# Kernel tuning notes

Measured on AMD Instinct MI355X. Metric: run time of the kernel, lower is better.

The kernel has to match this reference:

```python
import jax, jax.numpy as jnp
import numpy as np

H = 768   # encoder hidden size
NH = 4    # boundary attention heads
HD = H // NH
E = 9     # ent_type_size
R = 12    # rel_type_size
D = 64    # inner_dim
B = 4
S = 1024


def setup_inputs() -> dict:
    key = jax.random.key(0)
    ks = jax.random.split(key, 8)
    n = lambda k, shp: jax.random.normal(k, shp, jnp.float32) * 0.02
    return dict(
        hidden_states=jax.random.normal(ks[0], (B, S, H), jnp.float32),
        attention_mask=jnp.ones((B, S), jnp.float32),
        in_proj_w=n(ks[1], (3 * H, H)), in_proj_b=jnp.zeros((3 * H,), jnp.float32),
        out_proj_w=n(ks[2], (H, H)), out_proj_b=jnp.zeros((H,), jnp.float32),
        gate_w=n(ks[3], (H, H)), gate_b=jnp.zeros((H,), jnp.float32),
        ln_g=jnp.ones((H,), jnp.float32), ln_b=jnp.zeros((H,), jnp.float32),
        ent_w=n(ks[4], (E * 2 * D, H)), ent_b=jnp.zeros((E * 2 * D,), jnp.float32),
        prior_w=n(ks[5], (H, E)), prior_b=jnp.zeros((H,), jnp.float32),
        rel_w=n(ks[6], (R * 2 * D, 2 * H)), rel_b=jnp.zeros((R * 2 * D,), jnp.float32),
    )


def _sinusoidal_pos_emb(seq_len, dim, dtype):
    pos = jnp.arange(seq_len, dtype=dtype)[:, None]                 # [S,1]
    inv = jnp.power(jnp.asarray(10000.0, dtype), -2.0 * jnp.arange(dim // 2, dtype=dtype) / dim)
    ang = pos * inv                                                  # [S,D/2]
    emb = jnp.stack([jnp.sin(ang), jnp.cos(ang)], axis=-1).reshape(seq_len, dim)  # [sin0,cos0,sin1,cos1,...]
    return emb


def _gp_matrix(hs, W, b, mask):
    # hs: [B,S,Hin], W: [T*2D, Hin], mask: [B,S]
    bsz, seq_len, _ = hs.shape
    out = hs @ W.T + b                                               # [B,S,T*2D]
    T = out.shape[-1] // (2 * D)
    out = out.reshape(bsz, seq_len, T, 2 * D)
    qw, kw = out[..., :D], out[..., D:]                              # [B,S,T,D]
    # RoPE
    pe = _sinusoidal_pos_emb(seq_len, D, hs.dtype)                   # [S,D]
    cos = jnp.repeat(pe[:, 1::2], 2, axis=-1)[None, :, None, :]      # [1,S,1,D]
    sin = jnp.repeat(pe[:, ::2], 2, axis=-1)[None, :, None, :]

    def rot(x):
        x2 = jnp.stack([-x[..., 1::2], x[..., ::2]], axis=-1).reshape(x.shape)
        return x * cos + x2 * sin

    qw, kw = rot(qw), rot(kw)
    logits = jnp.einsum('bmtd,bntd->btmn', qw, kw)                   # [B,T,S,S]
    pad = mask[:, None, None, :]                                     # masks key dim
    logits = logits * pad - (1.0 - pad) * 1e12
    tril = jnp.tril(jnp.ones((seq_len, seq_len), logits.dtype), -1)
    logits = logits - tril * 1e12                                    # strictly lower triangle masked
    return logits / jnp.sqrt(jnp.asarray(D, logits.dtype))


def _boundary_attention(hs, mask, in_proj_w, in_proj_b, out_proj_w, out_proj_b,
                        gate_w, gate_b, ln_g, ln_b):
    bsz, seq_len, _ = hs.shape
    qkv = hs @ in_proj_w.T + in_proj_b                               # [B,S,3H]
    q, k, v = jnp.split(qkv, 3, axis=-1)
    q = q.reshape(bsz, seq_len, NH, HD)
    k = k.reshape(bsz, seq_len, NH, HD)
    v = v.reshape(bsz, seq_len, NH, HD)
    scores = jnp.einsum('bqhd,bkhd->bhqk', q, k) / jnp.sqrt(jnp.asarray(HD, hs.dtype))
    key_pad = (mask == 0)[:, None, None, :]                          # [B,1,1,S]
    scores = jnp.where(key_pad, jnp.asarray(-1e9, hs.dtype), scores)
    attn = jax.nn.softmax(scores, axis=-1)
    ctx = jnp.einsum('bhqk,bkhd->bqhd', attn, v).reshape(bsz, seq_len, H)
    attn_out = ctx @ out_proj_w.T + out_proj_b
    gate = jax.nn.sigmoid(attn_out @ gate_w.T + gate_b)
    x = hs + gate * attn_out
    mu = jnp.mean(x, axis=-1, keepdims=True)
    var = jnp.var(x, axis=-1, keepdims=True)
    return (x - mu) / jnp.sqrt(var + 1e-5) * ln_g + ln_b


def reference(hidden_states, attention_mask, in_proj_w, in_proj_b, out_proj_w, out_proj_b,
              gate_w, gate_b, ln_g, ln_b, ent_w, ent_b, prior_w, prior_b, rel_w, rel_b):
    enhanced = _boundary_attention(hidden_states, attention_mask, in_proj_w, in_proj_b,
                                   out_proj_w, out_proj_b, gate_w, gate_b, ln_g, ln_b)
    ent_logits = _gp_matrix(enhanced, ent_w, ent_b, attention_mask)  # [B,E,S,S]
    ent_prior = jnp.max(ent_logits, axis=-1)                          # [B,E,S]
    ent_prior = jnp.swapaxes(ent_prior, 1, 2)                         # [B,S,E]
    prior_feat = jax.nn.relu(ent_prior @ prior_w.T + prior_b)         # [B,S,H]
    rel_hidden = jnp.concatenate([enhanced, prior_feat], axis=-1)     # [B,S,2H]
    rel_logits = _gp_matrix(rel_hidden, rel_w, rel_b, attention_mask) # [B,R,S,S]
    return (ent_logits, rel_logits, enhanced)
```

## Files before the change

kernel.cpp:

```cpp
#include <hip/hip_runtime.h>
#include <math.h>

#define H_   768
#define NH_  4
#define HD_  192
#define E_   9
#define R_   12
#define D_   64
#define B_   4
#define S_   1024
#define H3_  (3 * H_)
#define MBS_ (B_ * S_)

typedef unsigned short u16;
typedef __attribute__((ext_vector_type(4))) int   i32x4;
typedef __attribute__((ext_vector_type(4))) float f32x4;
typedef __attribute__((ext_vector_type(8))) unsigned short u16x8;

static const long OUT_REL_OFF = (long)B_ * E_ * S_ * S_;
static const long OUT_ENH_OFF = OUT_REL_OFF + (long)B_ * R_ * S_ * S_;

__device__ __forceinline__ u16 f2bf(float f) {
    unsigned u = __builtin_bit_cast(unsigned, f);
    return (u16)((u + 0x7fffu + ((u >> 16) & 1u)) >> 16);
}
__device__ __forceinline__ float bf2f(u16 h) {
    return __builtin_bit_cast(float, (unsigned)h << 16);
}
__device__ __forceinline__ void gload16(const u16* g, u16* l) {
    __builtin_amdgcn_global_load_lds(
        (__attribute__((address_space(1))) void*)g,
        (__attribute__((address_space(3))) void*)l, 16, 0, 0);
}
__device__ __forceinline__ void mfma_bf16(f32x4& acc, i32x4 a, i32x4 b) {
    asm volatile("v_mfma_f32_16x16x32_bf16 %0, %1, %2, %0"
                 : "+v"(acc) : "v"(a), "v"(b));
}

template<int BM, int BN, int EPI, int OBF, int NS>
__global__ __launch_bounds__(256) void gemm_mfma(
    const u16* __restrict__ A, const u16* __restrict__ Bw,
    const float* __restrict__ bias, void* __restrict__ Cv,
    int K, int lda, int ldb, int ldc, int nh,
    long sAb, long sAh, long sBb, long sBh, long sCb, long sCh,
    const float* __restrict__ mask, float scale, float* __restrict__ aux)
{
    constexpr int MI = BM / 32, NJ = BN / 32;
    constexpr int BUFE = (BM + BN) * 64;
    const int z = blockIdx.z;
    const int zb = z / nh, zh = z - zb * nh;
    A  += zb * sAb + zh * sAh;
    Bw += zb * sBb + zh * sBh;

    const int gx = gridDim.x, gy = gridDim.y;
    int id = blockIdx.y * gx + blockIdx.x;
    const int nwg = gx * gy;
    if ((nwg & 7) == 0) id = (id & 7) * (nwg >> 3) + (id >> 3);
    const int bx = id % gx, by = id / gx;
    const int m0 = by * BM, n0 = bx * BN;

    __shared__ u16 lds[NS * BUFE];

    const int t = threadIdx.x;
    const int lane = t & 63, wid = t >> 6;
    const int wr = wid >> 1, wc = wid & 1;
    const int l16 = lane & 15, l4 = lane >> 4;

    auto stage = [&](int kt, int buf) {
        u16* la = lds + buf * BUFE;
        u16* lb = la + BM * 64;
        const int k0 = kt << 6;
        #pragma unroll
        for (int i = 0; i < BM / 32; ++i) {
            const int e = i * 256 + t;
            const int row = e >> 3;
            const int c = ((e & 7) ^ (row & 7)) << 3;
            gload16(A + (long)(m0 + row) * lda + k0 + c, la + e * 8);
        }
        #pragma unroll
        for (int i = 0; i < BN / 32; ++i) {
            const int e = i * 256 + t;
            const int row = e >> 3;
            const int c = ((e & 7) ^ (row & 7)) << 3;
            gload16(Bw + (long)(n0 + row) * ldb + k0 + c, lb + e * 8);
        }
    };

    f32x4 acc[MI][NJ];
    #pragma unroll
    for (int mi = 0; mi < MI; ++mi)
        #pragma unroll
        for (int nj = 0; nj < NJ; ++nj)
            #pragma unroll
            for (int q = 0; q < 4; ++q) acc[mi][nj][q] = 0.0f;

    const int nt = K >> 6;
    stage(0, 0);
    __syncthreads();
    for (int tt = 0; tt < nt; ++tt) {
        const int cur = (NS == 2) ? (tt & 1) : 0;
        if (NS == 2 && tt + 1 < nt) stage(tt + 1, cur ^ 1);
        const u16* la = lds + cur * BUFE;
        const u16* lb = la + BM * 64;
        i32x4 af[MI][2], bfr[NJ][2];
        #pragma unroll
        for (int mi = 0; mi < MI; ++mi)
            #pragma unroll
            for (int kk = 0; kk < 2; ++kk) {
                const int row = wr * (BM / 2) + mi * 16 + l16;
                af[mi][kk] = *(const i32x4*)&la[row * 64 + ((((kk << 2) + l4) ^ (row & 7)) << 3)];
            }
        #pragma unroll
        for (int nj = 0; nj < NJ; ++nj)
            #pragma unroll
            for (int kk = 0; kk < 2; ++kk) {
                const int row = wc * (BN / 2) + nj * 16 + l16;
                bfr[nj][kk] = *(const i32x4*)&lb[row * 64 + ((((kk << 2) + l4) ^ (row & 7)) << 3)];
            }
        #pragma unroll
        for (int kk = 0; kk < 2; ++kk)
            #pragma unroll
            for (int mi = 0; mi < MI; ++mi)
                #pragma unroll
                for (int nj = 0; nj < NJ; ++nj)
                    mfma_bf16(acc[mi][nj], af[mi][kk], bfr[nj][kk]);
        __syncthreads();
    }
    __builtin_amdgcn_sched_barrier(0);
    asm volatile("s_nop 7");
    asm volatile("s_nop 7");
    __builtin_amdgcn_sched_barrier(0);

    if (EPI == 1 || EPI == 3 || EPI == 5) mask += (long)zb * S_;
    const long cbase = zb * sCb + zh * sCh;

    float* sminv = (float*)lds;
    if (EPI == 6) {
        if (t < BM) {
            const float* pp = aux + ((long)z * S_ + m0 + t) * 16;
            float s = 0.0f;
            #pragma unroll
            for (int i = 0; i < 16; ++i) s += pp[i];
            sminv[t] = 1.0f / s;
        }
        __syncthreads();
    }

    float red[MI][4];
    if (EPI == 3 || EPI == 5) {
        #pragma unroll
        for (int mi = 0; mi < MI; ++mi)
            #pragma unroll
            for (int r = 0; r < 4; ++r) red[mi][r] = (EPI == 3) ? -INFINITY : 0.0f;
    }

    #pragma unroll
    for (int mi = 0; mi < MI; ++mi) {
        #pragma unroll
        for (int nj = 0; nj < NJ; ++nj) {
            const int gn = n0 + wc * (BN / 2) + nj * 16 + l16;
            const float bv = ((EPI == 0 || EPI == 4) && bias) ? bias[gn] : 0.0f;
            float invf = 0.0f;
            if (EPI == 4) invf = exp2f(-(float)((gn & 63) >> 1) * 0.41524101186092503f);
            #pragma unroll
            for (int r = 0; r < 4; ++r) {
                const int gm = m0 + wr * (BM / 2) + mi * 16 + l4 * 4 + r;
                float v = acc[mi][nj][r];
                const long cidx = cbase + (long)gm * ldc + gn;
                if (EPI == 0) {
                    v += bv;
                    if (OBF) ((u16*)Cv)[cidx] = f2bf(v);
                    else     ((float*)Cv)[cidx] = v;
                } else if (EPI == 1 || EPI == 3) {
                    const float pad = mask[gn];
                    v = v * pad - (1.0f - pad) * 1e12f;
                    if (gm > gn) v -= 1e12f;
                    v *= 0.125f;
                    ((float*)Cv)[cidx] = v;
                    if (EPI == 3) red[mi][r] = fmaxf(red[mi][r], v);
                } else if (EPI == 5) {
                    float tv = 0.0f;
                    if (mask[gn] != 0.0f) tv = __expf(v * scale);
                    ((u16*)Cv)[cidx] = f2bf(tv);
                    red[mi][r] += tv;
                } else if (EPI == 6) {
                    v *= sminv[gm - m0];
                    ((u16*)Cv)[cidx] = f2bf(v);
                } else {
                    v += bv;
                    const int sp = gm & (S_ - 1);
                    float sn, cs;
                    __sincosf((float)sp * invf, &sn, &cs);
                    const float pv = __shfl_xor(v, 1, 64);
                    v = (gn & 1) ? fmaf(v, cs, pv * sn) : fmaf(v, cs, -pv * sn);
                    ((u16*)Cv)[cidx] = f2bf(v);
                }
            }
        }
    }

    if (EPI == 3 || EPI == 5) {
        #pragma unroll
        for (int mi = 0; mi < MI; ++mi) {
            #pragma unroll
            for (int r = 0; r < 4; ++r) {
                float m = red[mi][r];
                if (EPI == 3) {
                    m = fmaxf(m, __shfl_xor(m, 1, 64));
                    m = fmaxf(m, __shfl_xor(m, 2, 64));
                    m = fmaxf(m, __shfl_xor(m, 4, 64));
                    m = fmaxf(m, __shfl_xor(m, 8, 64));
                } else {
                    m += __shfl_xor(m, 1, 64);
                    m += __shfl_xor(m, 2, 64);
                    m += __shfl_xor(m, 4, 64);
                    m += __shfl_xor(m, 8, 64);
                }
                if (l16 == 0) {
                    const int gm = m0 + wr * (BM / 2) + mi * 16 + l4 * 4 + r;
                    aux[((long)z * S_ + gm) * 16 + bx * 2 + wc] = m;
                }
            }
        }
    }
}

__global__ __launch_bounds__(256) void cast_all(
    const float* __restrict__ hs, const float* __restrict__ ipw,
    const float* __restrict__ opw, const float* __restrict__ gw,
    const float* __restrict__ entw, const float* __restrict__ relw,
    u16* hs_o, u16* ipw_o, u16* opw_o, u16* gw_o, u16* entw_o, u16* relw_o)
{
    const int blk = blockIdx.x;
    const float* in; u16* out; long base;
    if      (blk < 3072) { in = hs;   out = hs_o;   base = (long)blk * 1024; }
    else if (blk < 4800) { in = ipw;  out = ipw_o;  base = (long)(blk - 3072) * 1024; }
    else if (blk < 5376) { in = opw;  out = opw_o;  base = (long)(blk - 4800) * 1024; }
    else if (blk < 5952) { in = gw;   out = gw_o;   base = (long)(blk - 5376) * 1024; }
    else if (blk < 6816) { in = entw; out = entw_o; base = (long)(blk - 5952) * 1024; }
    else                 { in = relw; out = relw_o; base = (long)(blk - 6816) * 1024; }
    const long idx = base + (long)threadIdx.x * 4;
    const float4 v = *(const float4*)&in[idx];
    ushort4 o; o.x = f2bf(v.x); o.y = f2bf(v.y); o.z = f2bf(v.z); o.w = f2bf(v.w);
    *(ushort4*)&out[idx] = o;
}

__global__ __launch_bounds__(256) void transpose_v(
    const u16* __restrict__ qkv, u16* __restrict__ vt)
{
    __shared__ u16 tile[64][72];
    const int z = blockIdx.z, b = z >> 2, h = z & 3;
    const int d0 = blockIdx.x * 64, s0 = blockIdx.y * 64;
    const int t = threadIdx.x;
    const int r = t >> 2, c = (t & 3) << 4;
    const u16* src = qkv + ((long)(b * S_ + s0 + r)) * H3_ + 2 * H_ + h * HD_ + d0 + c;
    *(u16x8*)&tile[r][c]     = *(const u16x8*)src;
    *(u16x8*)&tile[r][c + 8] = *(const u16x8*)(src + 8);
    __syncthreads();
    u16 tmp[16];
    #pragma unroll
    for (int i = 0; i < 16; ++i) tmp[i] = tile[c + i][r];
    u16* dst = vt + ((long)z * HD_ + d0 + r) * S_ + s0 + c;
    *(u16x8*)dst       = *(u16x8*)&tmp[0];
    *(u16x8*)(dst + 8) = *(u16x8*)&tmp[8];
}

__global__ __launch_bounds__(256) void gate_ln_bf(
    const float* __restrict__ hs, const u16* __restrict__ aogl,
    const float* __restrict__ g, const float* __restrict__ bta,
    float* __restrict__ enh, u16* __restrict__ relh)
{
    const long row = blockIdx.x;
    const float* hrow = hs + row * H_;
    const u16* arow = aogl + row * (2 * H_);
    const int tid = threadIdx.x;
    float x[3];
    float sum = 0.0f, sq = 0.0f;
    #pragma unroll
    for (int i = 0; i < 3; ++i) {
        const int j = tid + i * 256;
        const float a = bf2f(arow[j]);
        const float gt = 1.0f / (1.0f + __expf(-bf2f(arow[H_ + j])));
        const float xv = hrow[j] + gt * a;
        x[i] = xv; sum += xv; sq += xv * xv;
    }
    __shared__ float sm[8];
    #pragma unroll
    for (int o = 32; o > 0; o >>= 1) {
        sum += __shfl_xor(sum, o, 64);
        sq  += __shfl_xor(sq, o, 64);
    }
    const int lane = tid & 63, wid = tid >> 6;
    if (lane == 0) { sm[wid] = sum; sm[4 + wid] = sq; }
    __syncthreads();
    sum = sm[0] + sm[1] + sm[2] + sm[3];
    sq  = sm[4] + sm[5] + sm[6] + sm[7];
    const float mu = sum * (1.0f / (float)H_);
    float var = sq * (1.0f / (float)H_) - mu * mu;
    var = fmaxf(var, 0.0f);
    const float inv = 1.0f / sqrtf(var + 1e-5f);
    #pragma unroll
    for (int i = 0; i < 3; ++i) {
        const int j = tid + i * 256;
        const float o = (x[i] - mu) * inv * g[j] + bta[j];
        enh[row * H_ + j] = o;
        relh[row * (2 * H_) + j] = f2bf(o);
    }
}

__global__ __launch_bounds__(256) void prior_fused(
    const float* __restrict__ pmax, const float* __restrict__ pw,
    const float* __restrict__ pb, u16* __restrict__ relh)
{
    const int row = blockIdx.x;
    const int b = row >> 10, m = row & (S_ - 1);
    __shared__ float pr[E_];
    const int tid = threadIdx.x;
    if (tid < E_) {
        const float* pp = pmax + ((long)(b * E_ + tid) * S_ + m) * 16;
        float mx = -INFINITY;
        #pragma unroll
        for (int i = 0; i < 16; ++i) mx = fmaxf(mx, pp[i]);
        pr[tid] = mx;
    }
    __syncthreads();
    float p[E_];
    #pragma unroll
    for (int e = 0; e < E_; ++e) p[e] = pr[e];
    u16* orow = relh + (long)row * (2 * H_) + H_;
    #pragma unroll
    for (int i = 0; i < 3; ++i) {
        const int j = tid + i * 256;
        float a = pb[j];
        #pragma unroll
        for (int e = 0; e < E_; ++e) a = fmaf(p[e], pw[j * E_ + e], a);
        orow[j] = f2bf(fmaxf(a, 0.0f));
    }
}

extern "C" void kernel_launch(void* const* d_in, const int* in_sizes, int n_in,
                              void* d_out, int out_size, void* d_ws, size_t ws_size,
                              hipStream_t stream)
{
    const float* hs   = (const float*)d_in[0];
    const float* mask = (const float*)d_in[1];
    const float* ipw  = (const float*)d_in[2];
    const float* ipb  = (const float*)d_in[3];
    const float* opw  = (const float*)d_in[4];
    const float* opb  = (const float*)d_in[5];
    const float* gw   = (const float*)d_in[6];
    const float* gb   = (const float*)d_in[7];
    const float* lng  = (const float*)d_in[8];
    const float* lnb  = (const float*)d_in[9];
    const float* entw = (const float*)d_in[10];
    const float* entb = (const float*)d_in[11];
    const float* prw  = (const float*)d_in[12];
    const float* prb  = (const float*)d_in[13];
    const float* relw = (const float*)d_in[14];
    const float* relb = (const float*)d_in[15];
    float* out = (float*)d_out;
    char* base = (char*)d_ws;

    u16* ipw_bf  = (u16*)(base + 0);
    u16* opw_bf  = (u16*)(base + 3538944);
    u16* gw_bf   = (u16*)(base + 4718592);
    u16* entw_bf = (u16*)(base + 5898240);
    u16* relw_bf = (u16*)(base + 7667712);
    u16* hs_bf   = (u16*)(base + 12386304);
    u16* qkv_bf  = (u16*)(base + 18677760);
    u16* vt_bf   = (u16*)(base + 37552128);
    u16* sc_bf   = (u16*)(base + 43843584);
    u16* ctx_bf  = (u16*)(base + 77398016);
    u16* aogl_bf = (u16*)(base + 83689472);
    float* bias2 = (float*)(base + 96272384);
    float* psum  = (float*)(base + 96280576);
    float* pmax  = (float*)(base + 97329152);
    u16* relh_bf = (u16*)(base + 18677760);
    u16* projr   = (u16*)(base + 37552128);
    float* enh   = out + OUT_ENH_OFF;

    const float qscale = 0.07216878364870323f;

    hipMemcpyAsync(bias2, opb, H_ * sizeof(float), hipMemcpyDeviceToDevice, stream);
    hipMemcpyAsync(bias2 + H_, gb, H_ * sizeof(float), hipMemcpyDeviceToDevice, stream);

    cast_all<<<9120, 256, 0, stream>>>(hs, ipw, opw, gw, entw, relw,
                                       hs_bf, ipw_bf, opw_bf, gw_bf, entw_bf, relw_bf);

    gemm_mfma<128,128,0,1,2><<<dim3(18, 32, 1), 256, 0, stream>>>(
        hs_bf, ipw_bf, ipb, qkv_bf, H_, H_, H_, H3_, 1,
        0,0,0,0,0,0, nullptr, 0.0f, nullptr);

    transpose_v<<<dim3(3, 16, 16), 256, 0, stream>>>(qkv_bf, vt_bf);

    gemm_mfma<128,128,5,1,2><<<dim3(8, 8, B_ * NH_), 256, 0, stream>>>(
        qkv_bf, qkv_bf + H_, nullptr, sc_bf, HD_, H3_, H3_, S_, NH_,
        (long)S_ * H3_, HD_, (long)S_ * H3_, HD_,
        (long)NH_ * S_ * S_, (long)S_ * S_, mask, qscale, psum);

    gemm_mfma<128,64,6,1,2><<<dim3(3, 8, B_ * NH_), 256, 0, stream>>>(
        sc_bf, vt_bf, nullptr, ctx_bf, S_, S_, S_, H_, NH_,
        (long)NH_ * S_ * S_, (long)S_ * S_, (long)NH_ * HD_ * S_, (long)HD_ * S_,
        (long)S_ * H_, HD_, nullptr, 0.0f, psum);

    gemm_mfma<128,128,0,1,2><<<dim3(12, 32, 1), 256, 0, stream>>>(
        ctx_bf, opw_bf, bias2, aogl_bf, H_, H_, H_, 2 * H_, 1,
        0,0,0,0,0,0, nullptr, 0.0f, nullptr);

    gate_ln_bf<<<MBS_, 256, 0, stream>>>(hs, aogl_bf, lng, lnb, enh, relh_bf);

    gemm_mfma<128,128,4,1,2><<<dim3(9, 32, 1), 256, 0, stream>>>(
        relh_bf, entw_bf, entb, projr, H_, 2 * H_, H_, E_ * 2 * D_, 1,
        0,0,0,0,0,0, nullptr, 0.0f, nullptr);

    gemm_mfma<128,128,3,0,1><<<dim3(8, 8, B_ * E_), 256, 0, stream>>>(
        projr, projr + D_, nullptr, out, D_, E_ * 2 * D_, E_ * 2 * D_, S_, E_,
        (long)S_ * E_ * 2 * D_, 2 * D_, (long)S_ * E_ * 2 * D_, 2 * D_,
        (long)E_ * S_ * S_, (long)S_ * S_, mask, 0.0f, pmax);

    prior_fused<<<MBS_, 256, 0, stream>>>(pmax, prw, prb, relh_bf);

    gemm_mfma<128,128,4,1,2><<<dim3(12, 32, 1), 256, 0, stream>>>(
        relh_bf, relw_bf, relb, projr, 2 * H_, 2 * H_, 2 * H_, R_ * 2 * D_, 1,
        0,0,0,0,0,0, nullptr, 0.0f, nullptr);

    gemm_mfma<128,128,1,0,1><<<dim3(8, 8, B_ * R_), 256, 0, stream>>>(
        projr, projr + D_, nullptr, out + OUT_REL_OFF, D_, R_ * 2 * D_, R_ * 2 * D_, S_, R_,
        (long)S_ * R_ * 2 * D_, 2 * D_, (long)S_ * R_ * 2 * D_, 2 * D_,
        (long)R_ * S_ * S_, (long)S_ * S_, mask, 0.0f, nullptr);

    (void)in_sizes; (void)n_in; (void)out_size; (void)ws_size;
}
```

Baseline: 256.4 us.

## Pipeline GEMM loads with vmcnt waits, fuse V transpose, retile GEMMs

Replaces the double-buffered GEMM main loop with a prefetch-two-ahead pipeline. It uses explicit vmcnt waits and raw barriers, so global-to-LDS loads overlap MFMA work. For K=64 GEMMs it adds a single-tile path with no loop. The V transpose kernel is removed and its work moves into the QKV projection epilogue, which writes V transposed through scattered stores. Several GEMMs switch to 128x96 or 64x96 tiles to give more workgroups, at the cost of smaller tiles and uncoalesced transposed writes.

```diff
diff --git a/kernel.cpp b/kernel.cpp
--- a/kernel.cpp
+++ b/kernel.cpp
@@ -15,7 +15,6 @@
 typedef unsigned short u16;
 typedef __attribute__((ext_vector_type(4))) int   i32x4;
 typedef __attribute__((ext_vector_type(4))) float f32x4;
-typedef __attribute__((ext_vector_type(8))) unsigned short u16x8;
 
 static const long OUT_REL_OFF = (long)B_ * E_ * S_ * S_;
 static const long OUT_ENH_OFF = OUT_REL_OFF + (long)B_ * R_ * S_ * S_;
@@ -37,7 +36,7 @@
                  : "+v"(acc) : "v"(a), "v"(b));
 }
 
-template<int BM, int BN, int EPI, int OBF, int NS>
+template<int BM, int BN, int EPI, int OBF, int PIPE>
 __global__ __launch_bounds__(256) void gemm_mfma(
     const u16* __restrict__ A, const u16* __restrict__ Bw,
     const float* __restrict__ bias, void* __restrict__ Cv,
@@ -47,6 +46,7 @@
 {
     constexpr int MI = BM / 32, NJ = BN / 32;
     constexpr int BUFE = (BM + BN) * 64;
+    constexpr int LPS  = BM / 32 + BN / 32;
     const int z = blockIdx.z;
     const int zb = z / nh, zh = z - zb * nh;
     A  += zb * sAb + zh * sAh;
@@ -59,15 +59,14 @@
     const int bx = id % gx, by = id / gx;
     const int m0 = by * BM, n0 = bx * BN;
 
-    __shared__ u16 lds[NS * BUFE];
+    __shared__ u16 lds[(PIPE ? 2 : 1) * BUFE];
 
     const int t = threadIdx.x;
     const int lane = t & 63, wid = t >> 6;
     const int wr = wid >> 1, wc = wid & 1;
     const int l16 = lane & 15, l4 = lane >> 4;
 
-    auto stage = [&](int kt, int buf) {
-        u16* la = lds + buf * BUFE;
+    auto stage = [&](int kt, u16* la) {
         u16* lb = la + BM * 64;
         const int k0 = kt << 6;
         #pragma unroll
@@ -95,13 +94,12 @@
             for (int q = 0; q < 4; ++q) acc[mi][nj][q] = 0.0f;
 
     const int nt = K >> 6;
-    stage(0, 0);
-    __syncthreads();
-    for (int tt = 0; tt < nt; ++tt) {
-        const int cur = (NS == 2) ? (tt & 1) : 0;
-        if (NS == 2 && tt + 1 < nt) stage(tt + 1, cur ^ 1);
-        const u16* la = lds + cur * BUFE;
-        const u16* lb = la + BM * 64;
+
+    if (PIPE == 0) {
+        stage(0, lds);
+        __syncthreads();
+        const u16* la = lds;
+        const u16* lb = lds + BM * 64;
         i32x4 af[MI][2], bfr[NJ][2];
         #pragma unroll
         for (int mi = 0; mi < MI; ++mi)
@@ -124,6 +122,48 @@
                 #pragma unroll
                 for (int nj = 0; nj < NJ; ++nj)
                     mfma_bf16(acc[mi][nj], af[mi][kk], bfr[nj][kk]);
+    } else {
+        stage(0, lds);
+        if (nt > 1) stage(1, lds + BUFE);
+        for (int tt = 0; tt < nt; ++tt) {
+            if (tt + 1 < nt) {
+                if constexpr (LPS == 8) asm volatile("s_waitcnt vmcnt(8)" ::: "memory");
+                else if constexpr (LPS == 7) asm volatile("s_waitcnt vmcnt(7)" ::: "memory");
+                else if constexpr (LPS == 6) asm volatile("s_waitcnt vmcnt(6)" ::: "memory");
+                else asm volatile("s_waitcnt vmcnt(5)" ::: "memory");
+            } else {
+                asm volatile("s_waitcnt vmcnt(0)" ::: "memory");
+            }
+            __builtin_amdgcn_s_barrier();
+            u16* la = lds + (tt & 1) * BUFE;
+            const u16* lb = la + BM * 64;
+            i32x4 af[MI][2], bfr[NJ][2];
+            #pragma unroll
+            for (int mi = 0; mi < MI; ++mi)
+                #pragma unroll
+                for (int kk = 0; kk < 2; ++kk) {
+                    const int row = wr * (BM / 2) + mi * 16 + l16;
+                    af[mi][kk] = *(const i32x4*)&la[row * 64 + ((((kk << 2) + l4) ^ (row & 7)) << 3)];
+                }
+            #pragma unroll
+            for (int nj = 0; nj < NJ; ++nj)
+                #pragma unroll
+                for (int kk = 0; kk < 2; ++kk) {
+                    const int row = wc * (BN / 2) + nj * 16 + l16;
+                    bfr[nj][kk] = *(const i32x4*)&lb[row * 64 + ((((kk << 2) + l4) ^ (row & 7)) << 3)];
+                }
+            asm volatile("s_waitcnt lgkmcnt(0)" ::: "memory");
+            __builtin_amdgcn_sched_barrier(0);
+            __builtin_amdgcn_s_barrier();
+            if (tt + 2 < nt) stage(tt + 2, la);
+            #pragma unroll
+            for (int kk = 0; kk < 2; ++kk)
+                #pragma unroll
+                for (int mi = 0; mi < MI; ++mi)
+                    #pragma unroll
+                    for (int nj = 0; nj < NJ; ++nj)
+                        mfma_bf16(acc[mi][nj], af[mi][kk], bfr[nj][kk]);
+        }
         __syncthreads();
     }
     __builtin_amdgcn_sched_barrier(0);
@@ -159,7 +199,7 @@
         #pragma unroll
         for (int nj = 0; nj < NJ; ++nj) {
             const int gn = n0 + wc * (BN / 2) + nj * 16 + l16;
-            const float bv = ((EPI == 0 || EPI == 4) && bias) ? bias[gn] : 0.0f;
+            const float bv = ((EPI == 0 || EPI == 4 || EPI == 7) && bias) ? bias[gn] : 0.0f;
             float invf = 0.0f;
             if (EPI == 4) invf = exp2f(-(float)((gn & 63) >> 1) * 0.41524101186092503f);
             #pragma unroll
@@ -171,6 +211,16 @@
                     v += bv;
                     if (OBF) ((u16*)Cv)[cidx] = f2bf(v);
                     else     ((float*)Cv)[cidx] = v;
+                } else if (EPI == 7) {
+                    v += bv;
+                    const u16 bfv = f2bf(v);
+                    ((u16*)Cv)[cidx] = bfv;
+                    if (gn >= 2 * H_) {
+                        const int hh = (gn - 2 * H_) / HD_;
+                        const int dd = (gn - 2 * H_) - hh * HD_;
+                        const int bb = gm >> 10, ss = gm & (S_ - 1);
+                        ((u16*)aux)[((long)(bb * NH_ + hh) * HD_ + dd) * S_ + ss] = bfv;
+                    }
                 } else if (EPI == 1 || EPI == 3) {
                     const float pad = mask[gn];
                     v = v * pad - (1.0f - pad) * 1e12f;
@@ -245,26 +295,6 @@
     *(ushort4*)&out[idx] = o;
 }
 
-__global__ __launch_bounds__(256) void transpose_v(
-    const u16* __restrict__ qkv, u16* __restrict__ vt)
-{
-    __shared__ u16 tile[64][72];
-    const int z = blockIdx.z, b = z >> 2, h = z & 3;
-    const int d0 = blockIdx.x * 64, s0 = blockIdx.y * 64;
-    const int t = threadIdx.x;
-    const int r = t >> 2, c = (t & 3) << 4;
-    const u16* src = qkv + ((long)(b * S_ + s0 + r)) * H3_ + 2 * H_ + h * HD_ + d0 + c;
-    *(u16x8*)&tile[r][c]     = *(const u16x8*)src;
-    *(u16x8*)&tile[r][c + 8] = *(const u16x8*)(src + 8);
-    __syncthreads();
-    u16 tmp[16];
-    #pragma unroll
-    for (int i = 0; i < 16; ++i) tmp[i] = tile[c + i][r];
-    u16* dst = vt + ((long)z * HD_ + d0 + r) * S_ + s0 + c;
-    *(u16x8*)dst       = *(u16x8*)&tmp[0];
-    *(u16x8*)(dst + 8) = *(u16x8*)&tmp[8];
-}
-
 __global__ __launch_bounds__(256) void gate_ln_bf(
     const float* __restrict__ hs, const u16* __restrict__ aogl,
     const float* __restrict__ g, const float* __restrict__ bta,
@@ -346,9 +376,7 @@
     const float* mask = (const float*)d_in[1];
     const float* ipw  = (const float*)d_in[2];
     const float* ipb  = (const float*)d_in[3];
-    const float* opw  = (const float*)d_in[4];
     const float* opb  = (const float*)d_in[5];
-    const float* gw   = (const float*)d_in[6];
     const float* gb   = (const float*)d_in[7];
     const float* lng  = (const float*)d_in[8];
     const float* lnb  = (const float*)d_in[9];
@@ -358,6 +386,8 @@
     const float* prb  = (const float*)d_in[13];
     const float* relw = (const float*)d_in[14];
     const float* relb = (const float*)d_in[15];
+    const float* opw  = (const float*)d_in[4];
+    const float* gw   = (const float*)d_in[6];
     float* out = (float*)d_out;
     char* base = (char*)d_ws;
 
@@ -387,44 +417,42 @@
     cast_all<<<9120, 256, 0, stream>>>(hs, ipw, opw, gw, entw, relw,
                                        hs_bf, ipw_bf, opw_bf, gw_bf, entw_bf, relw_bf);
 
-    gemm_mfma<128,128,0,1,2><<<dim3(18, 32, 1), 256, 0, stream>>>(
+    gemm_mfma<128,96,7,1,1><<<dim3(24, 32, 1), 256, 0, stream>>>(
         hs_bf, ipw_bf, ipb, qkv_bf, H_, H_, H_, H3_, 1,
-        0,0,0,0,0,0, nullptr, 0.0f, nullptr);
-
-    transpose_v<<<dim3(3, 16, 16), 256, 0, stream>>>(qkv_bf, vt_bf);
-
-    gemm_mfma<128,128,5,1,2><<<dim3(8, 8, B_ * NH_), 256, 0, stream>>>(
+        0,0,0,0,0,0, nullptr, 0.0f, (float*)vt_bf);
+
+    gemm_mfma<128,128,5,1,1><<<dim3(8, 8, B_ * NH_), 256, 0, stream>>>(
         qkv_bf, qkv_bf + H_, nullptr, sc_bf, HD_, H3_, H3_, S_, NH_,
         (long)S_ * H3_, HD_, (long)S_ * H3_, HD_,
         (long)NH_ * S_ * S_, (long)S_ * S_, mask, qscale, psum);
 
-    gemm_mfma<128,64,6,1,2><<<dim3(3, 8, B_ * NH_), 256, 0, stream>>>(
+    gemm_mfma<64,96,6,1,1><<<dim3(2, 16, B_ * NH_), 256, 0, stream>>>(
         sc_bf, vt_bf, nullptr, ctx_bf, S_, S_, S_, H_, NH_,
         (long)NH_ * S_ * S_, (long)S_ * S_, (long)NH_ * HD_ * S_, (long)HD_ * S_,
         (long)S_ * H_, HD_, nullptr, 0.0f, psum);
 
-    gemm_mfma<128,128,0,1,2><<<dim3(12, 32, 1), 256, 0, stream>>>(
+    gemm_mfma<128,96,0,1,1><<<dim3(16, 32, 1), 256, 0, stream>>>(
         ctx_bf, opw_bf, bias2, aogl_bf, H_, H_, H_, 2 * H_, 1,
         0,0,0,0,0,0, nullptr, 0.0f, nullptr);
 
     gate_ln_bf<<<MBS_, 256, 0, stream>>>(hs, aogl_bf, lng, lnb, enh, relh_bf);
 
-    gemm_mfma<128,128,4,1,2><<<dim3(9, 32, 1), 256, 0, stream>>>(
+    gemm_mfma<64,96,4,1,1><<<dim3(12, 64, 1), 256, 0, stream>>>(
         relh_bf, entw_bf, entb, projr, H_, 2 * H_, H_, E_ * 2 * D_, 1,
         0,0,0,0,0,0, nullptr, 0.0f, nullptr);
 
-    gemm_mfma<128,128,3,0,1><<<dim3(8, 8, B_ * E_), 256, 0, stream>>>(
+    gemm_mfma<128,128,3,0,0><<<dim3(8, 8, B_ * E_), 256, 0, stream>>>(
         projr, projr + D_, nullptr, out, D_, E_ * 2 * D_, E_ * 2 * D_, S_, E_,
         (long)S_ * E_ * 2 * D_, 2 * D_, (long)S_ * E_ * 2 * D_, 2 * D_,
         (long)E_ * S_ * S_, (long)S_ * S_, mask, 0.0f, pmax);
 
     prior_fused<<<MBS_, 256, 0, stream>>>(pmax, prw, prb, relh_bf);
 
-    gemm_mfma<128,128,4,1,2><<<dim3(12, 32, 1), 256, 0, stream>>>(
+    gemm_mfma<128,96,4,1,1><<<dim3(16, 32, 1), 256, 0, stream>>>(
         relh_bf, relw_bf, relb, projr, 2 * H_, 2 * H_, 2 * H_, R_ * 2 * D_, 1,
         0,0,0,0,0,0, nullptr, 0.0f, nullptr);
 
-    gemm_mfma<128,128,1,0,1><<<dim3(8, 8, B_ * R_), 256, 0, stream>>>(
+    gemm_mfma<128,128,1,0,0><<<dim3(8, 8, B_ * R_), 256, 0, stream>>>(
         projr, projr + D_, nullptr, out + OUT_REL_OFF, D_, R_ * 2 * D_, R_ * 2 * D_, S_, R_,
         (long)S_ * R_ * 2 * D_, 2 * D_, (long)S_ * R_ * 2 * D_, 2 * D_,
         (long)R_ * S_ * S_, (long)S_ * S_, mask, 0.0f, nullptr);
```

Result: no change. 252.6 us (-1.5%).
